# Optimization experiments

Measured on AMD Instinct MI355X. Metric: run time of the kernel, lower is better.

The kernel has to match this reference:

```python
import jax, jax.numpy as jnp
import numpy as np

IRREPS = [(32, 0), (16, 1), (8, 2)]          # (multiplicity, l)
DIMS = [m * (2 * l + 1) for m, l in IRREPS]  # [32, 48, 40]
OFF = np.concatenate([[0], np.cumsum(DIMS)]).astype(int)
FEAT = int(OFF[-1])                          # 120
H = 4                                        # num_heads
EPS = 1e-5
N_NODES = 50000
N_EDGES = 800000


def split(x):
    # split last axis into per-irrep blocks [..., mul, 2l+1]
    return [x[..., OFF[i]:OFF[i + 1]].reshape(x.shape[:-1] + (m, 2 * l + 1))
            for i, (m, l) in enumerate(IRREPS)]


def merge(blocks, lead):
    return jnp.concatenate([b.reshape(lead + (-1,)) for b in blocks], axis=-1)


def o3_linear(x, Ws):
    # e3nn o3.Linear: mixes multiplicities within each irrep type, 1/sqrt(fan_in) norm
    bs = split(x)
    out = [jnp.einsum('...im,io->...om', b, W) / np.sqrt(m)
           for b, W, (m, l) in zip(bs, Ws, IRREPS)]
    return merge(out, x.shape[:-1])


def norm_act(x):
    # e3nn nn.NormActivation with sigmoid: y = sigmoid(|x|) * x / |x| per irrep
    out = []
    for b in split(x):
        n = jnp.sqrt(jnp.sum(b * b, axis=-1, keepdims=True) + EPS * EPS)
        out.append(jax.nn.sigmoid(n) * b / n)
    return merge(out, x.shape[:-1])


def tp_dot(q, k, Wd):
    # FullyConnectedTensorProduct(q_ir, k_ir, 'Hx0e'), component normalization:
    # per-edge weighted inner products between matching irreps -> [E, H]
    fan = sum(m * m * (2 * l + 1) for m, l in IRREPS)
    out = 0.0
    for qb, kb, W, (m, l) in zip(split(q), split(k), Wd, IRREPS):
        out = out + jnp.einsum('eim,ejm,ijh->eh', qb, kb, W) / np.sqrt(2 * l + 1)
    return out / np.sqrt(fan)


def setup_inputs() -> dict:
    key = jax.random.key(0)
    ks = jax.random.split(key, 16)
    inp = {"node_features": jax.random.normal(ks[0], (N_NODES, FEAT), jnp.float32)}
    i = 1
    for name in ("Wq", "Wk", "Wv"):
        for j, (m, l) in enumerate(IRREPS):
            inp[f"{name}{j}"] = jax.random.normal(ks[i], (m, m), jnp.float32); i += 1
    for j, (m, l) in enumerate(IRREPS):
        inp[f"Wd{j}"] = jax.random.normal(ks[i], (m, m, H), jnp.float32); i += 1
    inp["edge_dst"] = jax.random.randint(ks[i], (N_EDGES,), 0, N_NODES); i += 1
    inp["edge_src"] = jax.random.randint(ks[i], (N_EDGES,), 0, N_NODES)
    return inp


def reference(node_features, Wq0, Wq1, Wq2, Wk0, Wk1, Wk2, Wv0, Wv1, Wv2,
              Wd0, Wd1, Wd2, edge_dst, edge_src):
    N = node_features.shape[0]
    q = norm_act(o3_linear(node_features, [Wq0, Wq1, Wq2]))              # [N, F]
    k = norm_act(o3_linear(node_features[edge_src], [Wk0, Wk1, Wk2]))    # [E, F]
    v_node = norm_act(o3_linear(node_features, [Wv0, Wv1, Wv2]))         # [N, F]
    v = v_node[edge_src]                                                 # [E, F]
    exp = jnp.exp(tp_dot(q[edge_dst], k, [Wd0, Wd1, Wd2]))               # [E, H]
    exp = jnp.mean(exp, axis=1, keepdims=True)                           # [E, 1]
    z = jax.ops.segment_sum(exp, edge_dst, num_segments=N)               # [N, 1]
    z = jnp.where(z == 0, 1.0, z)
    alpha = exp / z[edge_dst]                                            # [E, 1]
    f_out = jax.ops.segment_sum(jnp.sqrt(jax.nn.relu(alpha)) * v,
                                edge_dst, num_segments=N)                # [N, F]
    return f_out + v_node
```

## Files before the change

### kernel.cpp

```cpp
#include <hip/hip_runtime.h>
#include <math.h>

#define FEAT 120
#define HCNT 4

typedef unsigned short ushort_t;
typedef unsigned int uint_t;
typedef __attribute__((ext_vector_type(8))) short short8;
typedef __attribute__((ext_vector_type(4))) float floatx4;

__device__ __forceinline__ float nact_scale(float sumsq) {
    float n = sqrtf(sumsq + 1e-10f);
    float sig = 1.0f / (1.0f + expf(-n));
    return sig / n;
}

__device__ __forceinline__ ushort_t bf16r(float f) {
    uint_t u = __float_as_uint(f);
    u += 0x7fff + ((u >> 16) & 1);
    return (ushort_t)(u >> 16);
}

__device__ __forceinline__ uint_t pack2(float lo, float hi) {
    return (uint_t)bf16r(lo) | ((uint_t)bf16r(hi) << 16);
}

#define INV_S32 0.17677669529663687f
#define INV_S16 0.25f
#define INV_S8  0.35355339059327373f
#define S_IR0 0.02175970668223486f
#define S_IR1 0.012562972567021898f
#define S_IR2 0.009731317442393031f


__global__ __launch_bounds__(256) void zero_int_kernel(int* __restrict__ p, int n) {
    int i = blockIdx.x * 256 + threadIdx.x;
    if (i < n) p[i] = 0;
}

__global__ __launch_bounds__(256) void hist_kernel(const int* __restrict__ dst,
                                                   int* __restrict__ cnt, int E) {
    int e = blockIdx.x * 256 + threadIdx.x;
    if (e < E) atomicAdd(&cnt[dst[e]], 1);
}

__global__ __launch_bounds__(256) void scan_block_kernel(const int* __restrict__ cnt,
                                                         int* __restrict__ excl,
                                                         int* __restrict__ bsum, int n) {
    __shared__ int s[256];
    int t = threadIdx.x;
    int i = blockIdx.x * 256 + t;
    int v = (i < n) ? cnt[i] : 0;
    s[t] = v;
    __syncthreads();
    for (int off = 1; off < 256; off <<= 1) {
        int add = (t >= off) ? s[t - off] : 0;
        __syncthreads();
        s[t] += add;
        __syncthreads();
    }
    if (i < n) excl[i] = s[t] - v;
    if (t == 255) bsum[blockIdx.x] = s[255];
}

__global__ __launch_bounds__(256) void scan_sums_kernel(int* __restrict__ bsum, int nb) {
    __shared__ int s[256];
    int t = threadIdx.x;
    int v = (t < nb) ? bsum[t] : 0;
    s[t] = v;
    __syncthreads();
    for (int off = 1; off < 256; off <<= 1) {
        int add = (t >= off) ? s[t - off] : 0;
        __syncthreads();
        s[t] += add;
        __syncthreads();
    }
    if (t < nb) bsum[t] = s[t] - v;
}

__global__ __launch_bounds__(256) void add_offsets_kernel(int* __restrict__ offsets,
                                                          const int* __restrict__ bsum,
                                                          int* __restrict__ cursor,
                                                          int n, int E) {
    int i = blockIdx.x * 256 + threadIdx.x;
    if (i < n) {
        int off = offsets[i] + bsum[i >> 8];
        offsets[i] = off;
        cursor[i] = off;
    }
    if (i == 0) offsets[n] = E;
}

__global__ __launch_bounds__(256) void scatter_kernel(const int* __restrict__ dst,
                                                      const int* __restrict__ src,
                                                      int* __restrict__ cursor,
                                                      int* __restrict__ ssrc, int E) {
    int e = blockIdx.x * 256 + threadIdx.x;
    if (e < E) {
        int pos = atomicAdd(&cursor[dst[e]], 1);
        ssrc[pos] = src[e];
    }
}


__global__ __launch_bounds__(256) void prep_zero_kernel(uint_t* __restrict__ p, int nwords) {
    int i = blockIdx.x * 256 + threadIdx.x;
    if (i < nwords) p[i] = 0;
}

__global__ __launch_bounds__(256) void prep_fill_kernel(
    const float* __restrict__ Wq0, const float* __restrict__ Wq1, const float* __restrict__ Wq2,
    const float* __restrict__ Wk0, const float* __restrict__ Wk1, const float* __restrict__ Wk2,
    const float* __restrict__ Wv0, const float* __restrict__ Wv1, const float* __restrict__ Wv2,
    const float* __restrict__ Wd0, const float* __restrict__ Wd1, const float* __restrict__ Wd2,
    float* __restrict__ wt, ushort_t* __restrict__ wdtb)
{
    int t = threadIdx.x;
    for (int it = t; it < 3072; it += 256) {
        int p = it >> 10, rem = it & 1023, o = rem >> 5, i = rem & 31;
        const float* W = (p == 0) ? Wq0 : (p == 1) ? Wk0 : Wv0;
        wt[p * 1344 + o * 32 + i] = W[i * 32 + o] * INV_S32;
    }
    for (int it = t; it < 768; it += 256) {
        int p = it >> 8, rem = it & 255, o = rem >> 4, i = rem & 15;
        const float* W = (p == 0) ? Wq1 : (p == 1) ? Wk1 : Wv1;
        wt[p * 1344 + 1024 + o * 16 + i] = W[i * 16 + o] * INV_S16;
    }
    for (int it = t; it < 192; it += 256) {
        int p = it / 64, rem = it % 64, o = rem >> 3, i = rem & 7;
        const float* W = (p == 0) ? Wq2 : (p == 1) ? Wk2 : Wv2;
        wt[p * 1344 + 1280 + o * 8 + i] = W[i * 8 + o] * INV_S8;
    }
    for (int it = t; it < 4096; it += 256) {
        int i = it / 128, rem = it % 128, j = rem / 4, h = rem % 4;
        wdtb[(h * 128 + j) * 128 + i] = bf16r(Wd0[i * 128 + j * 4 + h] * S_IR0);
    }
    for (int it = t; it < 3072; it += 256) {
        int i = it / 192, rem = it % 192, j = rem / 12, r2 = rem % 12, c = r2 / 4, h = r2 % 4;
        wdtb[(h * 128 + 32 + j * 3 + c) * 128 + (32 + i * 3 + c)] = bf16r(Wd1[i * 64 + j * 4 + h] * S_IR1);
    }
    for (int it = t; it < 1280; it += 256) {
        int i = it / 160, rem = it % 160, j = rem / 20, r2 = rem % 20, c = r2 / 4, h = r2 % 4;
        wdtb[(h * 128 + 80 + j * 5 + c) * 128 + (80 + i * 5 + c)] = bf16r(Wd2[i * 32 + j * 4 + h] * S_IR2);
    }
}


__global__ __launch_bounds__(256) void node_qkv_v4_kernel(
    const float* __restrict__ x, const float* __restrict__ wt,
    ushort_t* __restrict__ qb, ushort_t* __restrict__ kb, ushort_t* __restrict__ vb, int N)
{
    int node = blockIdx.x * 256 + threadIdx.x;
    int p = blockIdx.y;
    int sec = blockIdx.z;
    if (node >= N) return;

    const float4* xp = (const float4*)(x + (size_t)node * FEAT);
    const float* W = wt + p * 1344;
    ushort_t* dstp = (p == 0) ? qb : (p == 1) ? kb : vb;
    uint4* dst = (uint4*)(dstp + (size_t)node * 128);

    if (sec == 0) {
        float xs[32];
        #pragma unroll
        for (int i = 0; i < 8; i++) ((float4*)xs)[i] = xp[i];
        uint_t yp[16];
        float prev = 0.0f;
        #pragma unroll
        for (int o = 0; o < 32; o++) {
            float acc = 0.0f;
            const float* w0 = W + o * 32;
            #pragma unroll
            for (int i = 0; i < 32; i++) acc = fmaf(w0[i], xs[i], acc);
            float y = acc * nact_scale(acc * acc);
            if (o & 1) yp[o >> 1] = pack2(prev, y); else prev = y;
        }
        #pragma unroll
        for (int i = 0; i < 4; i++)
            dst[i] = (uint4){yp[4*i], yp[4*i+1], yp[4*i+2], yp[4*i+3]};
    } else if (sec == 1) {
        float xs[48];
        #pragma unroll
        for (int i = 0; i < 12; i++) ((float4*)xs)[i] = xp[8 + i];
        uint_t yp[24];
        float prev = 0.0f;
        #pragma unroll
        for (int o = 0; o < 16; o++) {
            float a0 = 0.0f, a1 = 0.0f, a2 = 0.0f;
            const float* w1 = W + 1024 + o * 16;
            #pragma unroll
            for (int i = 0; i < 16; i++) {
                float w = w1[i];
                a0 = fmaf(w, xs[i * 3 + 0], a0);
                a1 = fmaf(w, xs[i * 3 + 1], a1);
                a2 = fmaf(w, xs[i * 3 + 2], a2);
            }
            float s = nact_scale(a0 * a0 + a1 * a1 + a2 * a2);
            float y0 = a0 * s, y1 = a1 * s, y2 = a2 * s;
            int f = o * 3;
            if (f & 1) {
                yp[f >> 1] = pack2(prev, y0);
                yp[(f >> 1) + 1] = pack2(y1, y2);
            } else {
                yp[f >> 1] = pack2(y0, y1);
                prev = y2;
            }
        }
        #pragma unroll
        for (int i = 0; i < 6; i++)
            dst[4 + i] = (uint4){yp[4*i], yp[4*i+1], yp[4*i+2], yp[4*i+3]};
    } else {
        float xs[40];
        #pragma unroll
        for (int i = 0; i < 10; i++) ((float4*)xs)[i] = xp[20 + i];
        uint_t yp[20];
        float prev = 0.0f;
        #pragma unroll
        for (int o = 0; o < 8; o++) {
            float a0 = 0, a1 = 0, a2 = 0, a3 = 0, a4 = 0;
            const float* w2 = W + 1280 + o * 8;
            #pragma unroll
            for (int i = 0; i < 8; i++) {
                float w = w2[i];
                a0 = fmaf(w, xs[i * 5 + 0], a0);
                a1 = fmaf(w, xs[i * 5 + 1], a1);
                a2 = fmaf(w, xs[i * 5 + 2], a2);
                a3 = fmaf(w, xs[i * 5 + 3], a3);
                a4 = fmaf(w, xs[i * 5 + 4], a4);
            }
            float s = nact_scale(a0*a0 + a1*a1 + a2*a2 + a3*a3 + a4*a4);
            float y0 = a0*s, y1 = a1*s, y2 = a2*s, y3 = a3*s, y4 = a4*s;
            int f = o * 5;
            if (f & 1) {
                yp[f >> 1] = pack2(prev, y0);
                yp[(f >> 1) + 1] = pack2(y1, y2);
                yp[(f >> 1) + 2] = pack2(y3, y4);
            } else {
                yp[f >> 1] = pack2(y0, y1);
                yp[(f >> 1) + 1] = pack2(y2, y3);
                prev = y4;
            }
        }
        #pragma unroll
        for (int i = 0; i < 5; i++)
            dst[10 + i] = (uint4){yp[4*i], yp[4*i+1], yp[4*i+2], yp[4*i+3]};
        dst[15] = (uint4){0, 0, 0, 0};
    }
}


__global__ __launch_bounds__(256, 2) void node_tq_mfma_kernel(
    const ushort_t* __restrict__ qb, const ushort_t* __restrict__ wdtb,
    ushort_t* __restrict__ tqb, int N)
{
    int t = threadIdx.x, lane = t & 63, w = t >> 6;
    int base = blockIdx.x * 16;
    int nl = lane & 15, quad = lane >> 4;
    int node = base + nl;
    int nclamp = (node < N) ? node : (N - 1);

    short8 bfr[4];
    const ushort_t* bp = qb + (size_t)nclamp * 128 + quad * 8;
    #pragma unroll
    for (int kk = 0; kk < 4; kk++) bfr[kk] = *(const short8*)(bp + kk * 32);

    #pragma unroll
    for (int ti = 0; ti < 8; ti++) {
        int tile = w * 8 + ti;
        const ushort_t* ap = wdtb + (tile * 16 + nl) * 128 + quad * 8;
        floatx4 C = {0.0f, 0.0f, 0.0f, 0.0f};
        #pragma unroll
        for (int kk = 0; kk < 4; kk++) {
            short8 a = *(const short8*)(ap + kk * 32);
            C = __builtin_amdgcn_mfma_f32_16x16x32_bf16(a, bfr[kk], C, 0, 0, 0);
        }
        if (node < N) {
            uint_t lo = (uint_t)bf16r(C[0]) | ((uint_t)bf16r(C[1]) << 16);
            uint_t hi = (uint_t)bf16r(C[2]) | ((uint_t)bf16r(C[3]) << 16);
            uint_t* dst = (uint_t*)(tqb + (size_t)node * 512 + tile * 16 + quad * 4);
            dst[0] = lo; dst[1] = hi;
        }
    }
}


__global__ __launch_bounds__(256) void edge_mfma_kernel(
    const ushort_t* __restrict__ tqb, const ushort_t* __restrict__ kb,
    const ushort_t* __restrict__ vb,
    const int* __restrict__ offsets, const int* __restrict__ ssrc,
    float* __restrict__ out, int N)
{
    int lane = threadIdx.x & 63, wid = threadIdx.x >> 6;
    int node = blockIdx.x * 4 + wid;
    if (node >= N) return;
    node = __builtin_amdgcn_readfirstlane(node);
    int m = lane & 15, quad = lane >> 4;

    short8 afr[4];
    if (m < HCNT) {
        const short8* ap = (const short8*)(tqb + (size_t)node * 512 + m * 128 + quad * 8);
        #pragma unroll
        for (int b = 0; b < 4; b++) afr[b] = ap[b * 4];
    } else {
        #pragma unroll
        for (int b = 0; b < 4; b++) afr[b] = (short8){0,0,0,0,0,0,0,0};
    }

    int beg = offsets[node], end = offsets[node + 1];
    float zpart = 0.0f, accx = 0.0f, accy = 0.0f;
    const uint_t* vrow = (const uint_t*)vb;

    for (int tb = beg; tb < end; tb += 16) {
        int rem = end - tb; if (rem > 16) rem = 16;
        int idx = tb + (m < rem ? m : rem - 1);
        int src = ssrc[idx];
        const short8* bp = (const short8*)(kb + (size_t)src * 128 + quad * 8);
        short8 b0 = bp[0], b1 = bp[4], b2 = bp[8], b3 = bp[12];
        floatx4 C = {0.0f, 0.0f, 0.0f, 0.0f};
        C = __builtin_amdgcn_mfma_f32_16x16x32_bf16(afr[0], b0, C, 0, 0, 0);
        C = __builtin_amdgcn_mfma_f32_16x16x32_bf16(afr[1], b1, C, 0, 0, 0);
        C = __builtin_amdgcn_mfma_f32_16x16x32_bf16(afr[2], b2, C, 0, 0, 0);
        C = __builtin_amdgcn_mfma_f32_16x16x32_bf16(afr[3], b3, C, 0, 0, 0);

        float w = 0.0f;
        if (quad == 0 && m < rem) {
            float ex = 0.25f * (__expf(C[0]) + __expf(C[1]) + __expf(C[2]) + __expf(C[3]));
            zpart += ex;
            w = sqrtf(ex);
        }

        if (rem == 16) {
            #pragma unroll
            for (int e0 = 0; e0 < 16; e0 += 8) {
                float we[8]; int se[8]; uint_t vp[8];
                #pragma unroll
                for (int j = 0; j < 8; j++) {
                    we[j] = __shfl(w, e0 + j, 64);
                    se[j] = __shfl(src, e0 + j, 64);
                }
                #pragma unroll
                for (int j = 0; j < 8; j++) vp[j] = vrow[(size_t)se[j] * 64 + lane];
                #pragma unroll
                for (int j = 0; j < 8; j++) {
                    accx = fmaf(we[j], __uint_as_float(vp[j] << 16), accx);
                    accy = fmaf(we[j], __uint_as_float(vp[j] & 0xffff0000u), accy);
                }
            }
        } else {
            for (int e = 0; e < rem; e++) {
                float we = __shfl(w, e, 64);
                int   se = __shfl(src, e, 64);
                uint_t vp = vrow[(size_t)se * 64 + lane];
                accx = fmaf(we, __uint_as_float(vp << 16), accx);
                accy = fmaf(we, __uint_as_float(vp & 0xffff0000u), accy);
            }
        }
    }

    zpart += __shfl_xor(zpart, 1, 64);
    zpart += __shfl_xor(zpart, 2, 64);
    zpart += __shfl_xor(zpart, 4, 64);
    zpart += __shfl_xor(zpart, 8, 64);
    float zsum = __shfl(zpart, 0, 64);
    float scale = (zsum > 0.0f) ? rsqrtf(zsum) : 0.0f;

    if (lane < 60) {
        uint_t vself = vrow[(size_t)node * 64 + lane];
        float2 o;
        o.x = fmaf(accx, scale, __uint_as_float(vself << 16));
        o.y = fmaf(accy, scale, __uint_as_float(vself & 0xffff0000u));
        *((float2*)(out + (size_t)node * FEAT) + lane) = o;
    }
}


extern "C" void kernel_launch(void* const* d_in, const int* in_sizes, int n_in,
                              void* d_out, int out_size, void* d_ws, size_t ws_size,
                              hipStream_t stream) {
    const float* x   = (const float*)d_in[0];
    const float* Wq0 = (const float*)d_in[1];
    const float* Wq1 = (const float*)d_in[2];
    const float* Wq2 = (const float*)d_in[3];
    const float* Wk0 = (const float*)d_in[4];
    const float* Wk1 = (const float*)d_in[5];
    const float* Wk2 = (const float*)d_in[6];
    const float* Wv0 = (const float*)d_in[7];
    const float* Wv1 = (const float*)d_in[8];
    const float* Wv2 = (const float*)d_in[9];
    const float* Wd0 = (const float*)d_in[10];
    const float* Wd1 = (const float*)d_in[11];
    const float* Wd2 = (const float*)d_in[12];
    const int* edge_dst = (const int*)d_in[13];
    const int* edge_src = (const int*)d_in[14];
    float* out = (float*)d_out;

    int N = in_sizes[0] / FEAT;
    int E = in_sizes[13];

    ushort_t* kb   = (ushort_t*)d_ws;
    ushort_t* vb   = kb + (size_t)N * 128;
    ushort_t* qb   = vb + (size_t)N * 128;
    ushort_t* tqb  = qb + (size_t)N * 128;
    ushort_t* wdtb = tqb + (size_t)N * 512;
    float* wt      = (float*)(wdtb + 65536);
    int* offsets = (int*)(wt + 4032);
    int* cursor  = offsets + (N + 1);
    int* bsum    = cursor + N;
    int* ssrc    = bsum + 256;

    int NB = (N + 255) / 256;
    int EB = (E + 255) / 256;
    int NW = (N + 3) / 4;
    int NT = (N + 15) / 16;

    prep_zero_kernel<<<128, 256, 0, stream>>>((uint_t*)wdtb, 32768);
    prep_fill_kernel<<<1, 256, 0, stream>>>(Wq0, Wq1, Wq2, Wk0, Wk1, Wk2,
                                            Wv0, Wv1, Wv2, Wd0, Wd1, Wd2, wt, wdtb);

    zero_int_kernel<<<NB, 256, 0, stream>>>(cursor, N);
    hist_kernel<<<EB, 256, 0, stream>>>(edge_dst, cursor, E);
    scan_block_kernel<<<NB, 256, 0, stream>>>(cursor, offsets, bsum, N);
    scan_sums_kernel<<<1, 256, 0, stream>>>(bsum, NB);
    add_offsets_kernel<<<NB, 256, 0, stream>>>(offsets, bsum, cursor, N, E);
    scatter_kernel<<<EB, 256, 0, stream>>>(edge_dst, edge_src, cursor, ssrc, E);

    node_qkv_v4_kernel<<<dim3(NB, 3, 3), 256, 0, stream>>>(x, wt, qb, kb, vb, N);
    node_tq_mfma_kernel<<<NT, 256, 0, stream>>>(qb, wdtb, tqb, N);
    edge_mfma_kernel<<<NW, 256, 0, stream>>>(tqb, kb, vb, offsets, ssrc, out, N);
}
```

Before: 391.5 us.

## Split per-node q/k/v bf16 buffers into per-irrep planar arrays

```diff
diff --git a/kernel.cpp b/kernel.cpp
--- a/kernel.cpp
+++ b/kernel.cpp
@@ -146,9 +146,12 @@
 }
 
 
-__global__ __launch_bounds__(256) void node_qkv_v4_kernel(
+__global__ __launch_bounds__(256) void node_qkv_v5_kernel(
     const float* __restrict__ x, const float* __restrict__ wt,
-    ushort_t* __restrict__ qb, ushort_t* __restrict__ kb, ushort_t* __restrict__ vb, int N)
+    ushort_t* __restrict__ S0q, ushort_t* __restrict__ S1q, ushort_t* __restrict__ S2q,
+    ushort_t* __restrict__ S0k, ushort_t* __restrict__ S1k, ushort_t* __restrict__ S2k,
+    ushort_t* __restrict__ S0v, ushort_t* __restrict__ S1v, ushort_t* __restrict__ S2v,
+    int N)
 {
     int node = blockIdx.x * 256 + threadIdx.x;
     int p = blockIdx.y;
@@ -157,8 +160,6 @@
 
     const float4* xp = (const float4*)(x + (size_t)node * FEAT);
     const float* W = wt + p * 1344;
-    ushort_t* dstp = (p == 0) ? qb : (p == 1) ? kb : vb;
-    uint4* dst = (uint4*)(dstp + (size_t)node * 128);
 
     if (sec == 0) {
         float xs[32];
@@ -175,6 +176,8 @@
             float y = acc * nact_scale(acc * acc);
             if (o & 1) yp[o >> 1] = pack2(prev, y); else prev = y;
         }
+        ushort_t* D = (p == 0) ? S0q : (p == 1) ? S0k : S0v;
+        uint4* dst = (uint4*)(D + (size_t)node * 32);
         #pragma unroll
         for (int i = 0; i < 4; i++)
             dst[i] = (uint4){yp[4*i], yp[4*i+1], yp[4*i+2], yp[4*i+3]};
@@ -206,9 +209,11 @@
                 prev = y2;
             }
         }
+        ushort_t* D = (p == 0) ? S1q : (p == 1) ? S1k : S1v;
+        uint4* dst = (uint4*)(D + (size_t)node * 48);
         #pragma unroll
         for (int i = 0; i < 6; i++)
-            dst[4 + i] = (uint4){yp[4*i], yp[4*i+1], yp[4*i+2], yp[4*i+3]};
+            dst[i] = (uint4){yp[4*i], yp[4*i+1], yp[4*i+2], yp[4*i+3]};
     } else {
         float xs[40];
         #pragma unroll
@@ -241,33 +246,40 @@
                 prev = y4;
             }
         }
+        ushort_t* D = (p == 0) ? S2q : (p == 1) ? S2k : S2v;
+        uint4* dst = (uint4*)(D + (size_t)node * 48);
         #pragma unroll
         for (int i = 0; i < 5; i++)
-            dst[10 + i] = (uint4){yp[4*i], yp[4*i+1], yp[4*i+2], yp[4*i+3]};
-        dst[15] = (uint4){0, 0, 0, 0};
-    }
-}
+            dst[i] = (uint4){yp[4*i], yp[4*i+1], yp[4*i+2], yp[4*i+3]};
+        dst[5] = (uint4){0, 0, 0, 0};
+    }
+}
+
 
 
 __global__ __launch_bounds__(256, 2) void node_tq_mfma_kernel(
-    const ushort_t* __restrict__ qb, const ushort_t* __restrict__ wdtb,
+    const ushort_t* __restrict__ S0q, const ushort_t* __restrict__ S1q,
+    const ushort_t* __restrict__ S2q, const ushort_t* __restrict__ wdtb,
     ushort_t* __restrict__ tqb, int N)
 {
     int t = threadIdx.x, lane = t & 63, w = t >> 6;
     int base = blockIdx.x * 16;
-    int nl = lane & 15, quad = lane >> 4;
+    int nl = lane & 15, quad = lane >> 4, q8 = quad * 8;
     int node = base + nl;
     int nclamp = (node < N) ? node : (N - 1);
 
+    size_t r32 = (size_t)nclamp * 32, r48 = (size_t)nclamp * 48;
     short8 bfr[4];
-    const ushort_t* bp = qb + (size_t)nclamp * 128 + quad * 8;
-    #pragma unroll
-    for (int kk = 0; kk < 4; kk++) bfr[kk] = *(const short8*)(bp + kk * 32);
+    bfr[0] = *(const short8*)(S0q + r32 + q8);
+    bfr[1] = *(const short8*)(S1q + r48 + q8);
+    bfr[2] = (quad < 2) ? *(const short8*)(S1q + r48 + 32 + q8)
+                        : *(const short8*)(S2q + r48 + q8 - 16);
+    bfr[3] = *(const short8*)(S2q + r48 + 16 + q8);
 
     #pragma unroll
     for (int ti = 0; ti < 8; ti++) {
         int tile = w * 8 + ti;
-        const ushort_t* ap = wdtb + (tile * 16 + nl) * 128 + quad * 8;
+        const ushort_t* ap = wdtb + (tile * 16 + nl) * 128 + q8;
         floatx4 C = {0.0f, 0.0f, 0.0f, 0.0f};
         #pragma unroll
         for (int kk = 0; kk < 4; kk++) {
@@ -285,8 +297,11 @@
 
 
 __global__ __launch_bounds__(256) void edge_mfma_kernel(
-    const ushort_t* __restrict__ tqb, const ushort_t* __restrict__ kb,
-    const ushort_t* __restrict__ vb,
+    const ushort_t* __restrict__ tqb,
+    const ushort_t* __restrict__ S0k, const ushort_t* __restrict__ S1k,
+    const ushort_t* __restrict__ S2k,
+    const ushort_t* __restrict__ S0v, const ushort_t* __restrict__ S1v,
+    const ushort_t* __restrict__ S2v,
     const int* __restrict__ offsets, const int* __restrict__ ssrc,
     float* __restrict__ out, int N)
 {
@@ -294,11 +309,11 @@
     int node = blockIdx.x * 4 + wid;
     if (node >= N) return;
     node = __builtin_amdgcn_readfirstlane(node);
-    int m = lane & 15, quad = lane >> 4;
+    int m = lane & 15, quad = lane >> 4, q8 = quad * 8;
 
     short8 afr[4];
     if (m < HCNT) {
-        const short8* ap = (const short8*)(tqb + (size_t)node * 512 + m * 128 + quad * 8);
+        const short8* ap = (const short8*)(tqb + (size_t)node * 512 + m * 128 + q8);
         #pragma unroll
         for (int b = 0; b < 4; b++) afr[b] = ap[b * 4];
     } else {
@@ -306,16 +321,28 @@
         for (int b = 0; b < 4; b++) afr[b] = (short8){0,0,0,0,0,0,0,0};
     }
 
+    const ushort_t* c2base = (quad < 2) ? S1k : S2k;
+    int c2off = (quad < 2) ? 32 + q8 : q8 - 16;
+
+    const uint_t* vb0 = (const uint_t*)S0v;
+    const uint_t* vb1 = (const uint_t*)S1v;
+    const uint_t* vb2 = (const uint_t*)S2v;
+    const uint_t* vbase = (lane < 16) ? vb0 : (lane < 40) ? vb1 : vb2;
+    int vstride = (lane < 16) ? 16 : 24;
+    int voff = (lane < 16) ? lane : (lane < 40) ? lane - 16 : lane - 40;
+
     int beg = offsets[node], end = offsets[node + 1];
     float zpart = 0.0f, accx = 0.0f, accy = 0.0f;
-    const uint_t* vrow = (const uint_t*)vb;
 
     for (int tb = beg; tb < end; tb += 16) {
         int rem = end - tb; if (rem > 16) rem = 16;
         int idx = tb + (m < rem ? m : rem - 1);
         int src = ssrc[idx];
-        const short8* bp = (const short8*)(kb + (size_t)src * 128 + quad * 8);
-        short8 b0 = bp[0], b1 = bp[4], b2 = bp[8], b3 = bp[12];
+        size_t r32 = (size_t)src * 32, r48 = (size_t)src * 48;
+        short8 b0 = *(const short8*)(S0k + r32 + q8);
+        short8 b1 = *(const short8*)(S1k + r48 + q8);
+        short8 b2 = *(const short8*)(c2base + r48 + c2off);
+        short8 b3 = *(const short8*)(S2k + r48 + 16 + q8);
         floatx4 C = {0.0f, 0.0f, 0.0f, 0.0f};
         C = __builtin_amdgcn_mfma_f32_16x16x32_bf16(afr[0], b0, C, 0, 0, 0);
         C = __builtin_amdgcn_mfma_f32_16x16x32_bf16(afr[1], b1, C, 0, 0, 0);
@@ -339,7 +366,8 @@
                     se[j] = __shfl(src, e0 + j, 64);
                 }
                 #pragma unroll
-                for (int j = 0; j < 8; j++) vp[j] = vrow[(size_t)se[j] * 64 + lane];
+                for (int j = 0; j < 8; j++)
+                    vp[j] = vbase[(size_t)se[j] * vstride + voff];
                 #pragma unroll
                 for (int j = 0; j < 8; j++) {
                     accx = fmaf(we[j], __uint_as_float(vp[j] << 16), accx);
@@ -350,7 +378,7 @@
             for (int e = 0; e < rem; e++) {
                 float we = __shfl(w, e, 64);
                 int   se = __shfl(src, e, 64);
-                uint_t vp = vrow[(size_t)se * 64 + lane];
+                uint_t vp = vbase[(size_t)se * vstride + voff];
                 accx = fmaf(we, __uint_as_float(vp << 16), accx);
                 accy = fmaf(we, __uint_as_float(vp & 0xffff0000u), accy);
             }
@@ -365,7 +393,7 @@
     float scale = (zsum > 0.0f) ? rsqrtf(zsum) : 0.0f;
 
     if (lane < 60) {
-        uint_t vself = vrow[(size_t)node * 64 + lane];
+        uint_t vself = vbase[(size_t)node * vstride + voff];
         float2 o;
         o.x = fmaf(accx, scale, __uint_as_float(vself << 16));
         o.y = fmaf(accy, scale, __uint_as_float(vself & 0xffff0000u));
@@ -397,10 +425,16 @@
     int N = in_sizes[0] / FEAT;
     int E = in_sizes[13];
 
-    ushort_t* kb   = (ushort_t*)d_ws;
-    ushort_t* vb   = kb + (size_t)N * 128;
-    ushort_t* qb   = vb + (size_t)N * 128;
-    ushort_t* tqb  = qb + (size_t)N * 128;
+    ushort_t* S0q = (ushort_t*)d_ws;
+    ushort_t* S1q = S0q + (size_t)N * 32;
+    ushort_t* S2q = S1q + (size_t)N * 48;
+    ushort_t* S0k = S2q + (size_t)N * 48;
+    ushort_t* S1k = S0k + (size_t)N * 32;
+    ushort_t* S2k = S1k + (size_t)N * 48;
+    ushort_t* S0v = S2k + (size_t)N * 48;
+    ushort_t* S1v = S0v + (size_t)N * 32;
+    ushort_t* S2v = S1v + (size_t)N * 48;
+    ushort_t* tqb = S2v + (size_t)N * 48;
     ushort_t* wdtb = tqb + (size_t)N * 512;
     float* wt      = (float*)(wdtb + 65536);
     int* offsets = (int*)(wt + 4032);
@@ -424,7 +458,9 @@
     add_offsets_kernel<<<NB, 256, 0, stream>>>(offsets, bsum, cursor, N, E);
     scatter_kernel<<<EB, 256, 0, stream>>>(edge_dst, edge_src, cursor, ssrc, E);
 
-    node_qkv_v4_kernel<<<dim3(NB, 3, 3), 256, 0, stream>>>(x, wt, qb, kb, vb, N);
-    node_tq_mfma_kernel<<<NT, 256, 0, stream>>>(qb, wdtb, tqb, N);
-    edge_mfma_kernel<<<NW, 256, 0, stream>>>(tqb, kb, vb, offsets, ssrc, out, N);
-}
+    node_qkv_v5_kernel<<<dim3(NB, 3, 3), 256, 0, stream>>>(
+        x, wt, S0q, S1q, S2q, S0k, S1k, S2k, S0v, S1v, S2v, N);
+    node_tq_mfma_kernel<<<NT, 256, 0, stream>>>(S0q, S1q, S2q, wdtb, tqb, N);
+    edge_mfma_kernel<<<NW, 256, 0, stream>>>(tqb, S0k, S1k, S2k, S0v, S1v, S2v,
+                                             offsets, ssrc, out, N);
+}
```

After: 407.3 us. 4.0% more time.
